# Kernel optimization log

Hardware: AMD Instinct MI355X
Metric: run time of the kernel (lower is better)

The kernel has to match this reference:

```python
import jax, jax.numpy as jnp
import numpy as np
import math

EPS_LN = 1e-5
TARGET_ACTIVITY = 0.1
THETA = 2.0 ** 16

B, NH, T, D, N = 2, 12, 2048, 768, 256


def layernorm(x):
    m = jnp.mean(x, axis=-1, keepdims=True)
    v = jnp.mean((x - m) ** 2, axis=-1, keepdims=True)
    return (x - m) / jnp.sqrt(v + EPS_LN)


def get_freqs(n):
    q = jnp.floor(jnp.arange(n, dtype=jnp.float32) / 2.0) * 2.0  # quantize by 2
    return 1.0 / (THETA ** (q / n)) / (2.0 * math.pi)


def rope(phases, v):
    ph = (phases % 1.0) * (2.0 * math.pi)
    c, s = jnp.cos(ph), jnp.sin(ph)
    even = v[..., 0::2]
    odd = v[..., 1::2]
    v_rot = jnp.stack((-odd, even), axis=-1).reshape(v.shape)  # interleaved rotate
    return v * c + v_rot * s


def setup_inputs() -> dict:
    key = jax.random.key(0)
    ks = jax.random.split(key, 5)
    std = 0.02
    return {
        "x": jax.random.normal(ks[0], (B, 1, T, D), dtype=jnp.float32),
        "encoder": jax.random.normal(ks[1], (NH, D, N), dtype=jnp.float32) * std,
        "encoder_v": jax.random.normal(ks[2], (NH, D, N), dtype=jnp.float32) * std,
        "decoder": jax.random.normal(ks[3], (NH * N, D), dtype=jnp.float32) * std,
        "scale": jnp.ones((D,), dtype=jnp.float32),
        "running_activity": jnp.ones((D,), dtype=jnp.float32) * TARGET_ACTIVITY,
    }


def reference(x, encoder, encoder_v, decoder, scale, running_activity):
    Bv, _, Tv, Dv = x.shape
    nh, _, Nv = encoder.shape

    # encode + ReLU sparsify: [B,1,T,D] @ [nh,D,N] -> [B,nh,T,N]
    x_latent = jnp.einsum('bztd,hdn->bhtn', x, encoder)
    x_sparse = jax.nn.relu(x_latent)

    # RoPE on Q=K=x_sparse
    freqs = get_freqs(Nv)  # [N]
    r_phases = jnp.arange(Tv, dtype=jnp.float32)[:, None] * freqs[None, :]  # [T,N]
    QR = rope(r_phases, x_sparse)
    KR = rope(r_phases, x_sparse)

    # non-softmax causal attention, strictly lower-triangular (diag=-1)
    scores = jnp.einsum('bhtn,bhsn->bhts', QR, KR)
    mask = jnp.tril(jnp.ones((Tv, Tv), dtype=scores.dtype), k=-1)
    scores = scores * mask
    yKV = jnp.einsum('bhts,bsd->bhtd', scores, x[:, 0])  # V = x

    yKV = layernorm(yKV)
    y_sparse = jax.nn.relu(jnp.einsum('bhtd,hdn->bhtn', yKV, encoder_v))
    xy_sparse = x_sparse * y_sparse  # [B,nh,T,N]; dropout=0 (eval)

    # [B,nh,T,N] -> [B,1,T,nh*N] @ [nh*N,D]
    flat = jnp.transpose(xy_sparse, (0, 2, 1, 3)).reshape(Bv, 1, Tv, nh * Nv)
    yMLP = flat @ decoder

    y = layernorm(yMLP)
    regulation = TARGET_ACTIVITY / (running_activity + 1e-6)
    y = y * jnp.sqrt(regulation) * scale

    return layernorm(x + y), xy_sparse
```

## Files before the change

kernel.cpp:

```cpp
#include <hip/hip_runtime.h>
#include <math.h>

#define TT 2048
#define DD 768
#define NN 256
#define NHH 12
#define BB 2
#define CH 512

typedef unsigned short u16;
typedef __attribute__((ext_vector_type(8))) short bf16x8;
typedef __attribute__((ext_vector_type(8))) unsigned short u16x8;
typedef __attribute__((ext_vector_type(4))) float f32x4;

static inline int imin(int a, int b) { return a < b ? a : b; }

__device__ __forceinline__ u16 f2b(float f) {
  union { float f; unsigned u; } a; a.f = f;
  unsigned r = a.u + 0x7FFF + ((a.u >> 16) & 1);
  return (u16)(r >> 16);
}
__device__ __forceinline__ float b2f(u16 h) {
  union { unsigned u; float f; } a; a.u = ((unsigned)h) << 16;
  return a.f;
}

__device__ __forceinline__ void async16(const void* g, void* l) {
  __builtin_amdgcn_global_load_lds(
      (const __attribute__((address_space(1))) unsigned*)g,
      (__attribute__((address_space(3))) unsigned*)l, 16, 0, 0);
}

__device__ __forceinline__ void stage128x32(
    const u16* __restrict__ gbase, size_t ld, u16* lds, int tid) {
  const int w = tid >> 6, l = tid & 63;
  const int r = l >> 2, kc = (l & 3) << 3;
#pragma unroll
  for (int q = 0; q < 2; ++q) {
    const int row0 = w * 32 + q * 16;
    async16(gbase + (size_t)(row0 + r) * ld + kc, lds + row0 * 32);
  }
}

__device__ __forceinline__ void stage64x32(
    const u16* __restrict__ gbase, size_t ld, u16* lds, int tid) {
  const int w = tid >> 6, l = tid & 63;
  const int r = w * 16 + (l >> 2), kc = (l & 3) << 3;
  async16(gbase + (size_t)r * ld + kc, lds + w * 512);
}

__device__ __forceinline__ void mfma_step(
    const u16* As, const u16* Bs, int wr, int wc, int lane, f32x4 acc[4][4]) {
  const int m16 = lane & 15, quad = lane >> 4;
  bf16x8 a[4], b[4];
#pragma unroll
  for (int i = 0; i < 4; ++i)
    a[i] = *(const bf16x8*)&As[(wr * 64 + i * 16 + m16) * 32 + quad * 8];
#pragma unroll
  for (int j = 0; j < 4; ++j)
    b[j] = *(const bf16x8*)&Bs[(wc * 64 + j * 16 + m16) * 32 + quad * 8];
#pragma unroll
  for (int i = 0; i < 4; ++i)
#pragma unroll
    for (int j = 0; j < 4; ++j)
      acc[i][j] = __builtin_amdgcn_mfma_f32_16x16x32_bf16(a[i], b[j], acc[i][j], 0, 0, 0);
}

__device__ __forceinline__ void copy_out64(
    const u16* buf, u16* g, size_t ld, int tid) {
#pragma unroll
  for (int s = 0; s < 4; ++s) {
    const int off = (s * 256 + tid) * 8;
    const int row = off >> 7, col = off & 127;
    *(u16x8*)&g[(size_t)row * ld + col] = *(const u16x8*)&buf[off];
  }
}

#define GEMM_PROLOGUE()                                            \
  __shared__ __attribute__((aligned(16))) u16 smem[16384];         \
  const int tid = threadIdx.x;                                     \
  const int w = tid >> 6, lane = tid & 63;                         \
  const int wr = w >> 1, wc = w & 1;                               \
  const int col16 = lane & 15, quad = lane >> 4;                   \
  f32x4 acc[4][4];                                                 \
  _Pragma("unroll") for (int i = 0; i < 4; ++i)                    \
  _Pragma("unroll") for (int j = 0; j < 4; ++j)                    \
      acc[i][j] = (f32x4){0.f, 0.f, 0.f, 0.f};

#define PIPELINED_K_LOOP(ABASE, ALD, BBASE, BLD, KTOT)                      \
  {                                                                         \
    u16* bA_ = smem; u16* bB_ = smem + 8192;                                \
    stage128x32((ABASE), (ALD), bA_, tid);                                  \
    stage128x32((BBASE), (BLD), bA_ + 4096, tid);                           \
    const int nk_ = (KTOT) / 32;                                            \
    for (int kp_ = 0; kp_ < nk_; ++kp_) {                                   \
      u16* cb_ = (kp_ & 1) ? bB_ : bA_;                                     \
      u16* nb_ = (kp_ & 1) ? bA_ : bB_;                                     \
      if (kp_ + 1 < nk_) {                                                  \
        const int kn_ = (kp_ + 1) * 32;                                     \
        stage128x32((ABASE) + kn_, (ALD), nb_, tid);                        \
        stage128x32((BBASE) + kn_, (BLD), nb_ + 4096, tid);                 \
        asm volatile("s_waitcnt vmcnt(4)" ::: "memory");                    \
      } else {                                                              \
        asm volatile("s_waitcnt vmcnt(0)" ::: "memory");                    \
      }                                                                     \
      __builtin_amdgcn_s_barrier();                                         \
      __builtin_amdgcn_sched_barrier(0);                                    \
      mfma_step(cb_, cb_ + 4096, wr, wc, lane, acc);                        \
      __builtin_amdgcn_sched_barrier(0);                                    \
      __builtin_amdgcn_s_barrier();                                         \
    }                                                                       \
  }

__global__ __launch_bounds__(256) void cvt_bf16(
    const float* __restrict__ in, u16* __restrict__ out, size_t n4) {
  size_t i = ((size_t)blockIdx.x * 256 + threadIdx.x) * 4;
  if (i >= n4 * 4) return;
  float4 v = *(const float4*)&in[i];
  u16 o[4] = {f2b(v.x), f2b(v.y), f2b(v.z), f2b(v.w)};
  *(ushort4*)&out[i] = *(ushort4*)o;
}

__global__ __launch_bounds__(256) void tcvt_bf16(
    const float* __restrict__ in, u16* __restrict__ out, int R, int C,
    size_t inStride, size_t outStride) {
  __shared__ float tile[32][33];
  const float* ip = in + (size_t)blockIdx.z * inStride;
  u16* op = out + (size_t)blockIdx.z * outStride;
  const int c0 = blockIdx.x * 32, r0 = blockIdx.y * 32;
  const int tx = threadIdx.x & 31, ty = threadIdx.x >> 5;
#pragma unroll
  for (int p = 0; p < 4; ++p)
    tile[ty + p * 8][tx] = ip[(size_t)(r0 + ty + p * 8) * C + c0 + tx];
  __syncthreads();
#pragma unroll
  for (int p = 0; p < 4; ++p)
    op[(size_t)(c0 + ty + p * 8) * R + r0 + tx] = f2b(tile[tx][ty + p * 8]);
}

__global__ __launch_bounds__(256) void k_colsum(
    const u16* __restrict__ encvt, float* __restrict__ colsum) {
  const int row = blockIdx.x * 4 + (threadIdx.x >> 6);
  const int lane = threadIdx.x & 63;
  const u16* pr = encvt + (size_t)row * DD;
  float s = 0.f;
#pragma unroll
  for (int i = 0; i < 3; ++i) {
    ushort4 v = *(const ushort4*)&pr[(lane << 2) + i * 256];
    s += b2f(v.x) + b2f(v.y) + b2f(v.z) + b2f(v.w);
  }
#pragma unroll
  for (int off = 32; off; off >>= 1) s += __shfl_xor(s, off);
  if (lane == 0) colsum[row] = s;
}

__global__ __launch_bounds__(256) void k1_encode(
    const u16* __restrict__ x16, const u16* __restrict__ enct,
    u16* __restrict__ qr16, u16* __restrict__ qrt16) {
  const int h = blockIdx.z;
  const int m0 = blockIdx.x * 128, n0 = blockIdx.y * 128;
  GEMM_PROLOGUE();
  PIPELINED_K_LOOP(x16 + (size_t)m0 * DD, DD,
                   enct + ((size_t)h * NN + n0) * DD, DD, DD);
#pragma unroll
  for (int p = 0; p < 2; ++p) {
    __syncthreads();
    if (wr == p) {
#pragma unroll
      for (int i = 0; i < 4; ++i)
#pragma unroll
        for (int j = 0; j < 4; ++j) {
          const int n = n0 + wc * 64 + j * 16 + col16;
          const int q = n & ~1;
          const float freq = exp2f((float)q * -0.0625f) * 0.15915494309189535f;
          float rv[4], pv[4];
#pragma unroll
          for (int r = 0; r < 4; ++r) rv[r] = fmaxf(acc[i][j][r], 0.f);
#pragma unroll
          for (int r = 0; r < 4; ++r) pv[r] = __shfl_xor(rv[r], 1);
#pragma unroll
          for (int r = 0; r < 4; ++r) {
            const int lr = i * 16 + quad * 4 + r;
            const int t = (m0 + p * 64 + lr) & (TT - 1);
            float phase = (float)t * freq;
            float ph = (phase - floorf(phase)) * 6.283185307179586f;
            float s = __sinf(ph), c = __cosf(ph);
            float o = (n & 1) ? (rv[r] * c + pv[r] * s) : (rv[r] * c - pv[r] * s);
            smem[lr * 128 + wc * 64 + j * 16 + col16] = f2b(o);
          }
        }
    }
    __syncthreads();
    const int m = m0 + p * 64;
    const int b = m >> 11, tb = m & (TT - 1);
    const size_t sl = (size_t)(b * NHH + h);
    copy_out64(smem, qr16 + (sl * TT + tb) * NN + n0, NN, tid);
#pragma unroll
    for (int s = 0; s < 4; ++s) {
      const int off = (s * 256 + tid) * 8;
      const int nr = off >> 6, tc = off & 63;
      u16 vals[8];
#pragma unroll
      for (int k = 0; k < 8; ++k) vals[k] = smem[(tc + k) * 128 + nr];
      *(u16x8*)&qrt16[(sl * NN + n0 + nr) * TT + tb + tc] = *(u16x8*)vals;
    }
  }
}

__global__ __launch_bounds__(256) void kS_band(
    const u16* __restrict__ qr16, u16* __restrict__ sb, int bh0) {
  const int z = blockIdx.y;
  const int bh = bh0 + z;
  const int cc = blockIdx.x / 10, rr = blockIdx.x % 10;
  int i = (int)((sqrtf(8.f * rr + 1.f) - 1.f) * 0.5f);
  while ((i + 1) * (i + 2) / 2 <= rr) ++i;
  while (i * (i + 1) / 2 > rr) --i;
  const int j = rr - i * (i + 1) / 2;
  const int t0 = (cc * 4 + i) * 128;
  const int s0 = cc * CH + j * 128;
  const u16* q = qr16 + (size_t)bh * TT * NN;
  GEMM_PROLOGUE();
  PIPELINED_K_LOOP(q + (size_t)t0 * NN, NN, q + (size_t)s0 * NN, NN, NN);
  const bool diag = (i == j);
#pragma unroll
  for (int p = 0; p < 2; ++p) {
    __syncthreads();
    if (wr == p) {
#pragma unroll
      for (int ii = 0; ii < 4; ++ii)
#pragma unroll
        for (int jj = 0; jj < 4; ++jj) {
          const int s = s0 + wc * 64 + jj * 16 + col16;
#pragma unroll
          for (int r = 0; r < 4; ++r) {
            const int lr = ii * 16 + quad * 4 + r;
            const int t = t0 + p * 64 + lr;
            float v = acc[ii][jj][r];
            if (diag && s >= t) v = 0.f;
            smem[lr * 128 + wc * 64 + jj * 16 + col16] = f2b(v);
          }
        }
    }
    __syncthreads();
    copy_out64(smem, sb + ((size_t)z * TT + t0 + p * 64) * CH + j * 128, CH, tid);
  }
}

__global__ __launch_bounds__(256) void kB_all(
    const u16* __restrict__ xt16, const u16* __restrict__ qrt16,
    u16* __restrict__ h16, int bh0) {
  __shared__ __attribute__((aligned(16))) u16 sm[20480];
  u16* buf0 = sm;
  u16* buf1 = sm + 6144;
  u16* snap = sm + 12288;
  const int tid = threadIdx.x;
  const int w = tid >> 6, lane = tid & 63;
  const int m16 = lane & 15, quad = lane >> 4;
  const int z = blockIdx.z;
  const int bh = bh0 + z, b = bh / NHH;
  const int d0 = blockIdx.x * 64, n0 = blockIdx.y * 128;
  f32x4 acc[4][2];
#pragma unroll
  for (int i = 0; i < 4; ++i)
#pragma unroll
    for (int j = 0; j < 2; ++j) acc[i][j] = (f32x4){0.f, 0.f, 0.f, 0.f};
  const u16* Ab = xt16 + ((size_t)b * DD + d0) * TT;
  const u16* Bb = qrt16 + ((size_t)bh * NN + n0) * TT;
  for (int c = 0; c < 3; ++c) {
    const int kbase = c * CH;
    stage64x32(Ab + kbase, TT, buf0, tid);
    stage128x32(Bb + kbase, TT, buf0 + 2048, tid);
    for (int s = 0; s < CH / 32; ++s) {
      u16* cb = (s & 1) ? buf1 : buf0;
      u16* nb = (s & 1) ? buf0 : buf1;
      if (s + 1 < CH / 32) {
        const int kn = kbase + (s + 1) * 32;
        stage64x32(Ab + kn, TT, nb, tid);
        stage128x32(Bb + kn, TT, nb + 2048, tid);
        asm volatile("s_waitcnt vmcnt(3)" ::: "memory");
      } else {
        asm volatile("s_waitcnt vmcnt(0)" ::: "memory");
      }
      __builtin_amdgcn_s_barrier();
      __builtin_amdgcn_sched_barrier(0);
      bf16x8 a[4], bb[2];
#pragma unroll
      for (int i = 0; i < 4; ++i)
        a[i] = *(const bf16x8*)&cb[(i * 16 + m16) * 32 + quad * 8];
#pragma unroll
      for (int j = 0; j < 2; ++j)
        bb[j] = *(const bf16x8*)&cb[2048 + (w * 32 + j * 16 + m16) * 32 + quad * 8];
#pragma unroll
      for (int i = 0; i < 4; ++i)
#pragma unroll
        for (int j = 0; j < 2; ++j)
          acc[i][j] = __builtin_amdgcn_mfma_f32_16x16x32_bf16(a[i], bb[j], acc[i][j], 0, 0, 0);
      __builtin_amdgcn_sched_barrier(0);
      __builtin_amdgcn_s_barrier();
    }
#pragma unroll
    for (int i = 0; i < 4; ++i)
#pragma unroll
      for (int j = 0; j < 2; ++j)
#pragma unroll
        for (int r = 0; r < 4; ++r)
          snap[(i * 16 + quad * 4 + r) * 128 + w * 32 + j * 16 + m16] =
              f2b(acc[i][j][r]);
    __syncthreads();
    u16* hd = h16 + (size_t)(z * 3 + c) * DD * NN;
#pragma unroll
    for (int s4 = 0; s4 < 4; ++s4) {
      const int off = (s4 * 256 + tid) * 8;
      const int row = off >> 7, col = off & 127;
      *(u16x8*)&hd[(size_t)(d0 + row) * NN + n0 + col] = *(const u16x8*)&snap[off];
    }
    __syncthreads();
  }
}

__device__ static const int TTORD[16] = {15, 11, 7, 14, 10, 6, 13, 9,
                                         5, 3, 12, 8, 4, 2, 1, 0};

__global__ __launch_bounds__(256) void kA_attn(
    const u16* __restrict__ qr16, const u16* __restrict__ h16,
    const u16* __restrict__ sb, const u16* __restrict__ xt16,
    u16* __restrict__ ykv16, int bh0) {
  __shared__ __attribute__((aligned(16))) u16 smem[32768];
  const int tid = threadIdx.x;
  const int w = tid >> 6, lane = tid & 63;
  const int wr = w >> 1, wc = w & 1;
  const int col16 = lane & 15, quad = lane >> 4;
  const int nwg = gridDim.x;
  const int bid = blockIdx.x;
  const int qq = nwg >> 3, r8 = nwg & 7;
  const int xcd = bid & 7, pos = bid >> 3;
  const int wg = (xcd < r8 ? xcd * (qq + 1) : r8 * (qq + 1) + (xcd - r8) * qq) + pos;
  const int z = wg / 96;
  const int tt = TTORD[(wg / 6) & 15];
  const int d0 = (wg % 6) * 128;
  const int bh = bh0 + z, b = bh / NHH;
  const int c = tt >> 2, it = tt & 3;
  const int t0 = tt * 128;
  f32x4 acc[4][4];
#pragma unroll
  for (int i = 0; i < 4; ++i)
#pragma unroll
    for (int j = 0; j < 4; ++j) acc[i][j] = (f32x4){0.f, 0.f, 0.f, 0.f};

  const int c4 = (c > 0) ? 4 : 0;
  const int nP = c4 + (it + 1) * 2;
  const u16* hs = h16 + ((size_t)(z * 3 + (c > 0 ? c - 1 : 0)) * DD + d0) * NN;
  const u16* qb = qr16 + ((size_t)bh * TT + t0) * NN;
  const u16* sbb = sb + ((size_t)z * TT + t0) * CH;
  const u16* xb = xt16 + ((size_t)b * DD + d0) * TT + c * CH;

#define KA_STAGE(buf, p)                                                  \
  {                                                                       \
    const u16 *pa_, *pb_; size_t la_, lb_;                                \
    if ((p) < c4) {                                                       \
      pa_ = qb + (p) * 64; la_ = NN;                                      \
      pb_ = hs + (p) * 64; lb_ = NN;                                      \
    } else {                                                              \
      const int q_ = (p) - c4;                                            \
      const int j_ = q_ >> 1, kk_ = (q_ & 1) << 6;                        \
      pa_ = sbb + j_ * 128 + kk_; la_ = CH;                               \
      pb_ = xb + j_ * 128 + kk_; lb_ = TT;                                \
    }                                                                     \
    stage128x32(pa_, la_, (buf), tid);                                    \
    stage128x32(pa_ + 32, la_, (buf) + 4096, tid);                        \
    stage128x32(pb_, lb_, (buf) + 8192, tid);                             \
    stage128x32(pb_ + 32, lb_, (buf) + 12288, tid);                       \
  }

  u16* bufA = smem;
  u16* bufB = smem + 16384;
  KA_STAGE(bufA, 0);
  for (int p = 0; p < nP; ++p) {
    u16* cb = (p & 1) ? bufB : bufA;
    u16* nb = (p & 1) ? bufA : bufB;
    if (p + 1 < nP) {
      KA_STAGE(nb, p + 1);
      asm volatile("s_waitcnt vmcnt(8)" ::: "memory");
    } else {
      asm volatile("s_waitcnt vmcnt(0)" ::: "memory");
    }
    __builtin_amdgcn_s_barrier();
    __builtin_amdgcn_sched_barrier(0);
    mfma_step(cb, cb + 8192, wr, wc, lane, acc);
    mfma_step(cb + 4096, cb + 12288, wr, wc, lane, acc);
    __builtin_amdgcn_sched_barrier(0);
    __builtin_amdgcn_s_barrier();
  }
#undef KA_STAGE

#pragma unroll
  for (int p = 0; p < 2; ++p) {
    __syncthreads();
    if (wr == p) {
#pragma unroll
      for (int i = 0; i < 4; ++i)
#pragma unroll
        for (int j = 0; j < 4; ++j)
#pragma unroll
          for (int r = 0; r < 4; ++r) {
            const int lr = i * 16 + quad * 4 + r;
            smem[lr * 128 + wc * 64 + j * 16 + col16] = f2b(acc[i][j][r]);
          }
    }
    __syncthreads();
    copy_out64(smem, ykv16 + ((size_t)z * TT + t0 + p * 64) * DD + d0, DD, tid);
  }
}

__global__ __launch_bounds__(256) void k3_stats(
    const u16* __restrict__ ykv16, float* __restrict__ mu, float* __restrict__ rs) {
  const int row = blockIdx.x * 4 + (threadIdx.x >> 6);
  const int lane = threadIdx.x & 63;
  const u16* p = ykv16 + (size_t)row * DD;
  float sum = 0.f, sq = 0.f;
#pragma unroll
  for (int i = 0; i < 3; ++i) {
    ushort4 v = *(const ushort4*)&p[(lane << 2) + i * 256];
    float f0 = b2f(v.x), f1 = b2f(v.y), f2 = b2f(v.z), f3 = b2f(v.w);
    sum += f0 + f1 + f2 + f3;
    sq += f0 * f0 + f1 * f1 + f2 * f2 + f3 * f3;
  }
#pragma unroll
  for (int off = 32; off; off >>= 1) {
    sum += __shfl_xor(sum, off);
    sq += __shfl_xor(sq, off);
  }
  if (lane == 0) {
    float m = sum * (1.f / 768.f);
    float v = sq * (1.f / 768.f) - m * m;
    mu[row] = m;
    rs[row] = rsqrtf(v + 1e-5f);
  }
}

__global__ __launch_bounds__(256) void k4_xy(
    const u16* __restrict__ ykv16, const u16* __restrict__ encvt,
    u16* __restrict__ qrxy, const float* __restrict__ mu,
    const float* __restrict__ rs, const float* __restrict__ colsum,
    float* __restrict__ out2, int bh0) {
  const int z = blockIdx.z;
  const int bh = bh0 + z, h = bh % NHH;
  const int t0 = blockIdx.x * 128, n0 = blockIdx.y * 128;
  GEMM_PROLOGUE();
  PIPELINED_K_LOOP(ykv16 + ((size_t)z * TT + t0) * DD, DD,
                   encvt + ((size_t)h * NN + n0) * DD, DD, DD);
#pragma unroll
  for (int p = 0; p < 2; ++p) {
    __syncthreads();
    if (wr == p) {
#pragma unroll
      for (int i = 0; i < 4; ++i)
#pragma unroll
        for (int j = 0; j < 4; ++j) {
          const int n = n0 + wc * 64 + j * 16 + col16;
          const int qn = n & ~1;
          const float freq = exp2f((float)qn * -0.0625f) * 0.15915494309189535f;
          const float cs = colsum[h * NN + n];
#pragma unroll
          for (int r = 0; r < 4; ++r) {
            const int lr = i * 16 + quad * 4 + r;
            const int t = t0 + p * 64 + lr;
            const int lrow = z * TT + t;
            const float muv = mu[lrow], rsv = rs[lrow];
            float ys = fmaxf(rsv * acc[i][j][r] - rsv * muv * cs, 0.f);
            const size_t gi = ((size_t)bh * TT + t) * NN + n;
            float qs = b2f(qrxy[gi]);
            float qp = b2f(qrxy[gi ^ 1]);
            float phase = (float)t * freq;
            float ph = (phase - floorf(phase)) * 6.283185307179586f;
            float s = __sinf(ph), c2 = __cosf(ph);
            float xs = (n & 1) ? (qs * c2 - qp * s) : (qs * c2 + qp * s);
            float val = ys * xs;
            out2[gi] = val;
            smem[lr * 128 + wc * 64 + j * 16 + col16] = f2b(val);
          }
        }
    }
    __syncthreads();
    copy_out64(smem, qrxy + ((size_t)bh * TT + t0 + p * 64) * NN + n0, NN, tid);
  }
}

__global__ __launch_bounds__(256) void k5_mlp(
    const u16* __restrict__ xyq, const u16* __restrict__ dect,
    float* __restrict__ ymlp) {
  __shared__ __attribute__((aligned(16))) u16 sm[8192];
  u16* buf0 = sm;
  u16* buf1 = sm + 4096;
  const int tid = threadIdx.x;
  const int w = tid >> 6, lane = tid & 63;
  const int wr = w >> 1, wc = w & 1;
  const int m16 = lane & 15, quad = lane >> 4;
  const int m0 = blockIdx.x * 64, d0 = blockIdx.y * 64;
  f32x4 acc[2][2];
#pragma unroll
  for (int i = 0; i < 2; ++i)
#pragma unroll
    for (int j = 0; j < 2; ++j) acc[i][j] = (f32x4){0.f, 0.f, 0.f, 0.f};
  const int ar = w * 16 + (lane >> 2);
  const int m = m0 + ar;
  const int b = m >> 11, t = m & (TT - 1);
  const int kc = (lane & 3) << 3;
  const int NK = NHH * NN / 32;
  async16(xyq + ((size_t)(b * NHH) * TT + t) * NN + kc, buf0 + w * 512);
  stage64x32(dect + (size_t)d0 * (NHH * NN), NHH * NN, buf0 + 2048, tid);
  for (int s = 0; s < NK; ++s) {
    u16* cb = (s & 1) ? buf1 : buf0;
    u16* nb = (s & 1) ? buf0 : buf1;
    if (s + 1 < NK) {
      const int k0 = (s + 1) * 32;
      const int hh = k0 >> 8;
      const int kk = (k0 & 255) + kc;
      async16(xyq + ((size_t)(b * NHH + hh) * TT + t) * NN + kk, nb + w * 512);
      stage64x32(dect + (size_t)d0 * (NHH * NN) + k0, NHH * NN, nb + 2048, tid);
      asm volatile("s_waitcnt vmcnt(2)" ::: "memory");
    } else {
      asm volatile("s_waitcnt vmcnt(0)" ::: "memory");
    }
    __builtin_amdgcn_s_barrier();
    __builtin_amdgcn_sched_barrier(0);
    bf16x8 a[2], bb[2];
#pragma unroll
    for (int i = 0; i < 2; ++i)
      a[i] = *(const bf16x8*)&cb[(wr * 32 + i * 16 + m16) * 32 + quad * 8];
#pragma unroll
    for (int j = 0; j < 2; ++j)
      bb[j] = *(const bf16x8*)&cb[2048 + (wc * 32 + j * 16 + m16) * 32 + quad * 8];
#pragma unroll
    for (int i = 0; i < 2; ++i)
#pragma unroll
      for (int j = 0; j < 2; ++j)
        acc[i][j] = __builtin_amdgcn_mfma_f32_16x16x32_bf16(a[i], bb[j], acc[i][j], 0, 0, 0);
    __builtin_amdgcn_sched_barrier(0);
    __builtin_amdgcn_s_barrier();
  }
#pragma unroll
  for (int i = 0; i < 2; ++i)
#pragma unroll
    for (int j = 0; j < 2; ++j) {
      const int d = d0 + wc * 32 + j * 16 + m16;
#pragma unroll
      for (int r = 0; r < 4; ++r) {
        const int mm = m0 + wr * 32 + i * 16 + quad * 4 + r;
        ymlp[(size_t)mm * DD + d] = acc[i][j][r];
      }
    }
}

__global__ __launch_bounds__(256) void k6_final(
    const float* __restrict__ ymlp, const float* __restrict__ x,
    const float* __restrict__ scale, const float* __restrict__ ra,
    float* __restrict__ out1) {
  const int row = blockIdx.x;
  const int tid = threadIdx.x;
  const int wid = tid >> 6, lane = tid & 63;
  __shared__ float red[8];
  float v[3];
  float sum = 0.f, sq = 0.f;
#pragma unroll
  for (int j = 0; j < 3; ++j) {
    v[j] = ymlp[(size_t)row * DD + tid + j * 256];
    sum += v[j]; sq += v[j] * v[j];
  }
#pragma unroll
  for (int off = 32; off; off >>= 1) { sum += __shfl_xor(sum, off); sq += __shfl_xor(sq, off); }
  if (lane == 0) { red[wid] = sum; red[4 + wid] = sq; }
  __syncthreads();
  sum = red[0] + red[1] + red[2] + red[3];
  sq = red[4] + red[5] + red[6] + red[7];
  const float m1 = sum * (1.f / 768.f);
  const float r1 = rsqrtf(sq * (1.f / 768.f) - m1 * m1 + 1e-5f);
  float z[3];
  float sum2 = 0.f, sq2 = 0.f;
#pragma unroll
  for (int j = 0; j < 3; ++j) {
    const int d = tid + j * 256;
    float y = (v[j] - m1) * r1 * sqrtf(0.1f / (ra[d] + 1e-6f)) * scale[d];
    z[j] = x[(size_t)row * DD + d] + y;
    sum2 += z[j]; sq2 += z[j] * z[j];
  }
  __syncthreads();
#pragma unroll
  for (int off = 32; off; off >>= 1) { sum2 += __shfl_xor(sum2, off); sq2 += __shfl_xor(sq2, off); }
  if (lane == 0) { red[wid] = sum2; red[4 + wid] = sq2; }
  __syncthreads();
  sum2 = red[0] + red[1] + red[2] + red[3];
  sq2 = red[4] + red[5] + red[6] + red[7];
  const float m2 = sum2 * (1.f / 768.f);
  const float r2 = rsqrtf(sq2 * (1.f / 768.f) - m2 * m2 + 1e-5f);
#pragma unroll
  for (int j = 0; j < 3; ++j)
    out1[(size_t)row * DD + tid + j * 256] = (z[j] - m2) * r2;
}

extern "C" void kernel_launch(void* const* d_in, const int* in_sizes, int n_in,
                              void* d_out, int out_size, void* d_ws, size_t ws_size,
                              hipStream_t stream) {
  const float* x = (const float*)d_in[0];
  const float* enc = (const float*)d_in[1];
  const float* encv = (const float*)d_in[2];
  const float* dec = (const float*)d_in[3];
  const float* scale = (const float*)d_in[4];
  const float* ra = (const float*)d_in[5];
  float* out1 = (float*)d_out;
  float* out2 = out1 + (size_t)BB * TT * DD;
  float* ymlp = out1;

  const int NS = BB * NHH;
  unsigned char* p = (unsigned char*)d_ws;
  u16* X16 = (u16*)p;    p += (size_t)BB * TT * DD * 2;
  u16* XT16 = (u16*)p;   p += (size_t)BB * DD * TT * 2;
  u16* ENCT = (u16*)p;   p += (size_t)NHH * NN * DD * 2;
  u16* ENCVT = (u16*)p;  p += (size_t)NHH * NN * DD * 2;
  u16* DECT = (u16*)p;   p += (size_t)DD * NHH * NN * 2;
  u16* QR16 = (u16*)p;   p += (size_t)NS * TT * NN * 2;
  u16* QRT16 = (u16*)p;  p += (size_t)NS * NN * TT * 2;
  float* COLSUM = (float*)p; p += (size_t)NHH * NN * 4;
  const size_t SLICE_B = (size_t)TT * CH * 2 + 3 * (size_t)DD * NN * 2 +
                         (size_t)TT * DD * 2 + (size_t)TT * 8;
  size_t fixed = (size_t)(p - (unsigned char*)d_ws);
  size_t rem = (ws_size > fixed) ? ws_size - fixed : 0;
  int GSmax = (int)(rem / SLICE_B);
  if (GSmax < 1) GSmax = 1;
  if (GSmax > NS) GSmax = NS;
  const int ngrp = (NS + GSmax - 1) / GSmax;
  const int GS = (NS + ngrp - 1) / ngrp;
  u16* SB = (u16*)p;     p += (size_t)GS * TT * CH * 2;
  u16* H16 = (u16*)p;    p += (size_t)GS * 3 * DD * NN * 2;
  u16* YKV16 = (u16*)p;  p += (size_t)GS * TT * DD * 2;
  float* MU = (float*)p; p += (size_t)GS * TT * 4;
  float* RS = (float*)p; p += (size_t)GS * TT * 4;

  cvt_bf16<<<dim3((BB * TT * DD) / 1024), 256, 0, stream>>>(x, X16, (size_t)BB * TT * DD / 4);
  tcvt_bf16<<<dim3(DD / 32, TT / 32, BB), 256, 0, stream>>>(
      x, XT16, TT, DD, (size_t)TT * DD, (size_t)DD * TT);
  tcvt_bf16<<<dim3(NN / 32, DD / 32, NHH), 256, 0, stream>>>(
      enc, ENCT, DD, NN, (size_t)DD * NN, (size_t)NN * DD);
  tcvt_bf16<<<dim3(NN / 32, DD / 32, NHH), 256, 0, stream>>>(
      encv, ENCVT, DD, NN, (size_t)DD * NN, (size_t)NN * DD);
  tcvt_bf16<<<dim3(DD / 32, (NHH * NN) / 32, 1), 256, 0, stream>>>(
      dec, DECT, NHH * NN, DD, 0, 0);
  k_colsum<<<dim3(NHH * NN / 4), 256, 0, stream>>>(ENCVT, COLSUM);

  k1_encode<<<dim3(BB * TT / 128, NN / 128, NHH), 256, 0, stream>>>(
      X16, ENCT, QR16, QRT16);

  for (int bh0 = 0; bh0 < NS; bh0 += GS) {
    const int gs = imin(GS, NS - bh0);
    kS_band<<<dim3(40, gs), 256, 0, stream>>>(QR16, SB, bh0);
    kB_all<<<dim3(DD / 64, NN / 128, gs), 256, 0, stream>>>(
        XT16, QRT16, H16, bh0);
    kA_attn<<<dim3(96 * gs), 256, 0, stream>>>(
        QR16, H16, SB, XT16, YKV16, bh0);
    k3_stats<<<dim3(gs * TT / 4), 256, 0, stream>>>(YKV16, MU, RS);
    k4_xy<<<dim3(TT / 128, NN / 128, gs), 256, 0, stream>>>(
        YKV16, ENCVT, QR16, MU, RS, COLSUM, out2, bh0);
  }

  k5_mlp<<<dim3(BB * TT / 64, DD / 64), 256, 0, stream>>>(QR16, DECT, ymlp);
  k6_final<<<dim3(BB * TT), 256, 0, stream>>>(ymlp, x, scale, ra, out1);
}
```

Before: 409.7 us.

## Precompute RoPE cos/sin table, single-pass epilogues, and K=64 staging in MLP GEMM

Adds a kernel that precomputes a cos/sin table per (t, pair). The encode and xy kernels now read this table instead of evaluating exp2/sin/cos per element. The two-pass half-tile epilogues in several GEMM kernels become one full 128-row smem pass with a single copy-out, which removes extra barriers. The MLP GEMM now stages 64-wide K chunks per iteration to halve the number of loop iterations and barriers. Other changes: packed pair loads of QR in k4 and hoisted mu/rs loads. The costs are one extra small kernel and a larger LDS footprint in k5.

```diff
diff --git a/kernel.cpp b/kernel.cpp
--- a/kernel.cpp
+++ b/kernel.cpp
@@ -66,10 +66,10 @@
       acc[i][j] = __builtin_amdgcn_mfma_f32_16x16x32_bf16(a[i], b[j], acc[i][j], 0, 0, 0);
 }
 
-__device__ __forceinline__ void copy_out64(
+__device__ __forceinline__ void copy_out128(
     const u16* buf, u16* g, size_t ld, int tid) {
 #pragma unroll
-  for (int s = 0; s < 4; ++s) {
+  for (int s = 0; s < 8; ++s) {
     const int off = (s * 256 + tid) * 8;
     const int row = off >> 7, col = off & 127;
     *(u16x8*)&g[(size_t)row * ld + col] = *(const u16x8*)&buf[off];
@@ -154,56 +154,57 @@
   if (lane == 0) colsum[row] = s;
 }
 
+__global__ __launch_bounds__(256) void k_cstab(float2* __restrict__ cs) {
+  const int idx = blockIdx.x * 256 + threadIdx.x;
+  const int t = idx >> 7, n2 = idx & 127;
+  const float freq = exp2f((float)(2 * n2) * -0.0625f) * 0.15915494309189535f;
+  const float phase = (float)t * freq;
+  const float ph = (phase - floorf(phase)) * 6.283185307179586f;
+  cs[idx] = make_float2(__cosf(ph), __sinf(ph));
+}
+
 __global__ __launch_bounds__(256) void k1_encode(
     const u16* __restrict__ x16, const u16* __restrict__ enct,
+    const float2* __restrict__ CS,
     u16* __restrict__ qr16, u16* __restrict__ qrt16) {
   const int h = blockIdx.z;
   const int m0 = blockIdx.x * 128, n0 = blockIdx.y * 128;
   GEMM_PROLOGUE();
   PIPELINED_K_LOOP(x16 + (size_t)m0 * DD, DD,
                    enct + ((size_t)h * NN + n0) * DD, DD, DD);
-#pragma unroll
-  for (int p = 0; p < 2; ++p) {
-    __syncthreads();
-    if (wr == p) {
-#pragma unroll
-      for (int i = 0; i < 4; ++i)
-#pragma unroll
-        for (int j = 0; j < 4; ++j) {
-          const int n = n0 + wc * 64 + j * 16 + col16;
-          const int q = n & ~1;
-          const float freq = exp2f((float)q * -0.0625f) * 0.15915494309189535f;
-          float rv[4], pv[4];
-#pragma unroll
-          for (int r = 0; r < 4; ++r) rv[r] = fmaxf(acc[i][j][r], 0.f);
-#pragma unroll
-          for (int r = 0; r < 4; ++r) pv[r] = __shfl_xor(rv[r], 1);
-#pragma unroll
-          for (int r = 0; r < 4; ++r) {
-            const int lr = i * 16 + quad * 4 + r;
-            const int t = (m0 + p * 64 + lr) & (TT - 1);
-            float phase = (float)t * freq;
-            float ph = (phase - floorf(phase)) * 6.283185307179586f;
-            float s = __sinf(ph), c = __cosf(ph);
-            float o = (n & 1) ? (rv[r] * c + pv[r] * s) : (rv[r] * c - pv[r] * s);
-            smem[lr * 128 + wc * 64 + j * 16 + col16] = f2b(o);
-          }
-        }
-    }
-    __syncthreads();
-    const int m = m0 + p * 64;
-    const int b = m >> 11, tb = m & (TT - 1);
-    const size_t sl = (size_t)(b * NHH + h);
-    copy_out64(smem, qr16 + (sl * TT + tb) * NN + n0, NN, tid);
-#pragma unroll
-    for (int s = 0; s < 4; ++s) {
-      const int off = (s * 256 + tid) * 8;
-      const int nr = off >> 6, tc = off & 63;
-      u16 vals[8];
-#pragma unroll
-      for (int k = 0; k < 8; ++k) vals[k] = smem[(tc + k) * 128 + nr];
-      *(u16x8*)&qrt16[(sl * NN + n0 + nr) * TT + tb + tc] = *(u16x8*)vals;
-    }
+  __syncthreads();
+#pragma unroll
+  for (int i = 0; i < 4; ++i)
+#pragma unroll
+    for (int j = 0; j < 4; ++j) {
+      const int n = n0 + wc * 64 + j * 16 + col16;
+      float rv[4], pv[4];
+#pragma unroll
+      for (int r = 0; r < 4; ++r) rv[r] = fmaxf(acc[i][j][r], 0.f);
+#pragma unroll
+      for (int r = 0; r < 4; ++r) pv[r] = __shfl_xor(rv[r], 1);
+#pragma unroll
+      for (int r = 0; r < 4; ++r) {
+        const int lrow = wr * 64 + i * 16 + quad * 4 + r;
+        const int t = (m0 + lrow) & (TT - 1);
+        const float2 cs = CS[t * 128 + (n >> 1)];
+        const float o = (n & 1) ? (rv[r] * cs.x + pv[r] * cs.y)
+                                : (rv[r] * cs.x - pv[r] * cs.y);
+        smem[lrow * 128 + wc * 64 + j * 16 + col16] = f2b(o);
+      }
+    }
+  __syncthreads();
+  const int bq = m0 >> 11, tb = m0 & (TT - 1);
+  const size_t sl = (size_t)(bq * NHH + h);
+  copy_out128(smem, qr16 + (sl * TT + tb) * NN + n0, NN, tid);
+#pragma unroll
+  for (int s = 0; s < 8; ++s) {
+    const int off = (s * 256 + tid) * 8;
+    const int nr = off >> 7, tc = off & 127;
+    u16 vals[8];
+#pragma unroll
+    for (int k = 0; k < 8; ++k) vals[k] = smem[(tc + k) * 128 + nr];
+    *(u16x8*)&qrt16[(sl * NN + n0 + nr) * TT + tb + tc] = *(u16x8*)vals;
   }
 }
 
@@ -222,28 +223,23 @@
   GEMM_PROLOGUE();
   PIPELINED_K_LOOP(q + (size_t)t0 * NN, NN, q + (size_t)s0 * NN, NN, NN);
   const bool diag = (i == j);
-#pragma unroll
-  for (int p = 0; p < 2; ++p) {
-    __syncthreads();
-    if (wr == p) {
-#pragma unroll
-      for (int ii = 0; ii < 4; ++ii)
-#pragma unroll
-        for (int jj = 0; jj < 4; ++jj) {
-          const int s = s0 + wc * 64 + jj * 16 + col16;
-#pragma unroll
-          for (int r = 0; r < 4; ++r) {
-            const int lr = ii * 16 + quad * 4 + r;
-            const int t = t0 + p * 64 + lr;
-            float v = acc[ii][jj][r];
-            if (diag && s >= t) v = 0.f;
-            smem[lr * 128 + wc * 64 + jj * 16 + col16] = f2b(v);
-          }
-        }
-    }
-    __syncthreads();
-    copy_out64(smem, sb + ((size_t)z * TT + t0 + p * 64) * CH + j * 128, CH, tid);
-  }
+  __syncthreads();
+#pragma unroll
+  for (int ii = 0; ii < 4; ++ii)
+#pragma unroll
+    for (int jj = 0; jj < 4; ++jj) {
+      const int s = s0 + wc * 64 + jj * 16 + col16;
+#pragma unroll
+      for (int r = 0; r < 4; ++r) {
+        const int lrow = wr * 64 + ii * 16 + quad * 4 + r;
+        const int t = t0 + lrow;
+        float v = acc[ii][jj][r];
+        if (diag && s >= t) v = 0.f;
+        smem[lrow * 128 + wc * 64 + jj * 16 + col16] = f2b(v);
+      }
+    }
+  __syncthreads();
+  copy_out128(smem, sb + ((size_t)z * TT + t0) * CH + j * 128, CH, tid);
 }
 
 __global__ __launch_bounds__(256) void kB_all(
@@ -393,23 +389,18 @@
   }
 #undef KA_STAGE
 
-#pragma unroll
-  for (int p = 0; p < 2; ++p) {
-    __syncthreads();
-    if (wr == p) {
-#pragma unroll
-      for (int i = 0; i < 4; ++i)
-#pragma unroll
-        for (int j = 0; j < 4; ++j)
-#pragma unroll
-          for (int r = 0; r < 4; ++r) {
-            const int lr = i * 16 + quad * 4 + r;
-            smem[lr * 128 + wc * 64 + j * 16 + col16] = f2b(acc[i][j][r]);
-          }
-    }
-    __syncthreads();
-    copy_out64(smem, ykv16 + ((size_t)z * TT + t0 + p * 64) * DD + d0, DD, tid);
-  }
+  __syncthreads();
+#pragma unroll
+  for (int i = 0; i < 4; ++i)
+#pragma unroll
+    for (int j = 0; j < 4; ++j)
+#pragma unroll
+      for (int r = 0; r < 4; ++r) {
+        const int lrow = wr * 64 + i * 16 + quad * 4 + r;
+        smem[lrow * 128 + wc * 64 + j * 16 + col16] = f2b(acc[i][j][r]);
+      }
+  __syncthreads();
+  copy_out128(smem, ykv16 + ((size_t)z * TT + t0) * DD + d0, DD, tid);
 }
 
 __global__ __launch_bounds__(256) void k3_stats(
@@ -440,6 +431,7 @@
 
 __global__ __launch_bounds__(256) void k4_xy(
     const u16* __restrict__ ykv16, const u16* __restrict__ encvt,
+    const float2* __restrict__ CS,
     u16* __restrict__ qrxy, const float* __restrict__ mu,
     const float* __restrict__ rs, const float* __restrict__ colsum,
     float* __restrict__ out2, int bh0) {
@@ -449,49 +441,47 @@
   GEMM_PROLOGUE();
   PIPELINED_K_LOOP(ykv16 + ((size_t)z * TT + t0) * DD, DD,
                    encvt + ((size_t)h * NN + n0) * DD, DD, DD);
-#pragma unroll
-  for (int p = 0; p < 2; ++p) {
-    __syncthreads();
-    if (wr == p) {
-#pragma unroll
-      for (int i = 0; i < 4; ++i)
-#pragma unroll
-        for (int j = 0; j < 4; ++j) {
-          const int n = n0 + wc * 64 + j * 16 + col16;
-          const int qn = n & ~1;
-          const float freq = exp2f((float)qn * -0.0625f) * 0.15915494309189535f;
-          const float cs = colsum[h * NN + n];
-#pragma unroll
-          for (int r = 0; r < 4; ++r) {
-            const int lr = i * 16 + quad * 4 + r;
-            const int t = t0 + p * 64 + lr;
-            const int lrow = z * TT + t;
-            const float muv = mu[lrow], rsv = rs[lrow];
-            float ys = fmaxf(rsv * acc[i][j][r] - rsv * muv * cs, 0.f);
-            const size_t gi = ((size_t)bh * TT + t) * NN + n;
-            float qs = b2f(qrxy[gi]);
-            float qp = b2f(qrxy[gi ^ 1]);
-            float phase = (float)t * freq;
-            float ph = (phase - floorf(phase)) * 6.283185307179586f;
-            float s = __sinf(ph), c2 = __cosf(ph);
-            float xs = (n & 1) ? (qs * c2 - qp * s) : (qs * c2 + qp * s);
-            float val = ys * xs;
-            out2[gi] = val;
-            smem[lr * 128 + wc * 64 + j * 16 + col16] = f2b(val);
-          }
-        }
-    }
-    __syncthreads();
-    copy_out64(smem, qrxy + ((size_t)bh * TT + t0 + p * 64) * NN + n0, NN, tid);
-  }
+  __syncthreads();
+#pragma unroll
+  for (int i = 0; i < 4; ++i) {
+    float muv[4], rsv[4];
+#pragma unroll
+    for (int r = 0; r < 4; ++r) {
+      const int lrow = z * TT + t0 + wr * 64 + i * 16 + quad * 4 + r;
+      muv[r] = mu[lrow];
+      rsv[r] = rs[lrow];
+    }
+#pragma unroll
+    for (int j = 0; j < 4; ++j) {
+      const int n = n0 + wc * 64 + j * 16 + col16;
+      const float csum = colsum[h * NN + n];
+#pragma unroll
+      for (int r = 0; r < 4; ++r) {
+        const int lrow = wr * 64 + i * 16 + quad * 4 + r;
+        const int t = t0 + lrow;
+        const float ys = fmaxf(rsv[r] * acc[i][j][r] - rsv[r] * muv[r] * csum, 0.f);
+        const size_t gi = ((size_t)bh * TT + t) * NN + n;
+        const unsigned pq = *(const unsigned*)&qrxy[gi & ~(size_t)1];
+        const float lo = b2f((u16)pq), hi = b2f((u16)(pq >> 16));
+        const float2 cs = CS[t * 128 + (n >> 1)];
+        const float xs = (n & 1) ? (hi * cs.x - lo * cs.y)
+                                 : (lo * cs.x + hi * cs.y);
+        const float val = ys * xs;
+        out2[gi] = val;
+        smem[lrow * 128 + wc * 64 + j * 16 + col16] = f2b(val);
+      }
+    }
+  }
+  __syncthreads();
+  copy_out128(smem, qrxy + ((size_t)bh * TT + t0) * NN + n0, NN, tid);
 }
 
 __global__ __launch_bounds__(256) void k5_mlp(
     const u16* __restrict__ xyq, const u16* __restrict__ dect,
     float* __restrict__ ymlp) {
-  __shared__ __attribute__((aligned(16))) u16 sm[8192];
+  __shared__ __attribute__((aligned(16))) u16 sm[16384];
   u16* buf0 = sm;
-  u16* buf1 = sm + 4096;
+  u16* buf1 = sm + 8192;
   const int tid = threadIdx.x;
   const int w = tid >> 6, lane = tid & 63;
   const int wr = w >> 1, wc = w & 1;
@@ -506,39 +496,50 @@
   const int m = m0 + ar;
   const int b = m >> 11, t = m & (TT - 1);
   const int kc = (lane & 3) << 3;
-  const int NK = NHH * NN / 32;
-  async16(xyq + ((size_t)(b * NHH) * TT + t) * NN + kc, buf0 + w * 512);
-  stage64x32(dect + (size_t)d0 * (NHH * NN), NHH * NN, buf0 + 2048, tid);
+#define K5_STAGE(buf, k0)                                                   \
+  {                                                                         \
+    const int hh_ = (k0) >> 8;                                              \
+    const int kk_ = ((k0) & 255) + kc;                                      \
+    const u16* ap_ = xyq + ((size_t)(b * NHH + hh_) * TT + t) * NN;         \
+    async16(ap_ + kk_, (buf) + w * 512);                                    \
+    async16(ap_ + kk_ + 32, (buf) + 2048 + w * 512);                        \
+    stage64x32(dect + (size_t)d0 * (NHH * NN) + (k0), NHH * NN,             \
+               (buf) + 4096, tid);                                          \
+    stage64x32(dect + (size_t)d0 * (NHH * NN) + (k0) + 32, NHH * NN,        \
+               (buf) + 6144, tid);                                          \
+  }
+  const int NK = (NHH * NN) / 64;
+  K5_STAGE(buf0, 0);
   for (int s = 0; s < NK; ++s) {
     u16* cb = (s & 1) ? buf1 : buf0;
     u16* nb = (s & 1) ? buf0 : buf1;
     if (s + 1 < NK) {
-      const int k0 = (s + 1) * 32;
-      const int hh = k0 >> 8;
-      const int kk = (k0 & 255) + kc;
-      async16(xyq + ((size_t)(b * NHH + hh) * TT + t) * NN + kk, nb + w * 512);
-      stage64x32(dect + (size_t)d0 * (NHH * NN) + k0, NHH * NN, nb + 2048, tid);
-      asm volatile("s_waitcnt vmcnt(2)" ::: "memory");
+      K5_STAGE(nb, (s + 1) * 64);
+      asm volatile("s_waitcnt vmcnt(4)" ::: "memory");
     } else {
       asm volatile("s_waitcnt vmcnt(0)" ::: "memory");
     }
     __builtin_amdgcn_s_barrier();
     __builtin_amdgcn_sched_barrier(0);
-    bf16x8 a[2], bb[2];
-#pragma unroll
-    for (int i = 0; i < 2; ++i)
-      a[i] = *(const bf16x8*)&cb[(wr * 32 + i * 16 + m16) * 32 + quad * 8];
-#pragma unroll
-    for (int j = 0; j < 2; ++j)
-      bb[j] = *(const bf16x8*)&cb[2048 + (wc * 32 + j * 16 + m16) * 32 + quad * 8];
-#pragma unroll
-    for (int i = 0; i < 2; ++i)
+#pragma unroll
+    for (int half = 0; half < 2; ++half) {
+      bf16x8 a[2], bb[2];
+#pragma unroll
+      for (int i = 0; i < 2; ++i)
+        a[i] = *(const bf16x8*)&cb[half * 2048 + (wr * 32 + i * 16 + m16) * 32 + quad * 8];
 #pragma unroll
       for (int j = 0; j < 2; ++j)
-        acc[i][j] = __builtin_amdgcn_mfma_f32_16x16x32_bf16(a[i], bb[j], acc[i][j], 0, 0, 0);
+        bb[j] = *(const bf16x8*)&cb[4096 + half * 2048 + (wc * 32 + j * 16 + m16) * 32 + quad * 8];
+#pragma unroll
+      for (int i = 0; i < 2; ++i)
+#pragma unroll
+        for (int j = 0; j < 2; ++j)
+          acc[i][j] = __builtin_amdgcn_mfma_f32_16x16x32_bf16(a[i], bb[j], acc[i][j], 0, 0, 0);
+    }
     __builtin_amdgcn_sched_barrier(0);
     __builtin_amdgcn_s_barrier();
   }
+#undef K5_STAGE
 #pragma unroll
   for (int i = 0; i < 2; ++i)
 #pragma unroll
@@ -621,6 +622,7 @@
   u16* QR16 = (u16*)p;   p += (size_t)NS * TT * NN * 2;
   u16* QRT16 = (u16*)p;  p += (size_t)NS * NN * TT * 2;
   float* COLSUM = (float*)p; p += (size_t)NHH * NN * 4;
+  float2* CS = (float2*)p;   p += (size_t)TT * (NN / 2) * sizeof(float2);
   const size_t SLICE_B = (size_t)TT * CH * 2 + 3 * (size_t)DD * NN * 2 +
                          (size_t)TT * DD * 2 + (size_t)TT * 8;
   size_t fixed = (size_t)(p - (unsigned char*)d_ws);
@@ -646,9 +648,10 @@
   tcvt_bf16<<<dim3(DD / 32, (NHH * NN) / 32, 1), 256, 0, stream>>>(
       dec, DECT, NHH * NN, DD, 0, 0);
   k_colsum<<<dim3(NHH * NN / 4), 256, 0, stream>>>(ENCVT, COLSUM);
+  k_cstab<<<dim3(TT * (NN / 2) / 256), 256, 0, stream>>>(CS);
 
   k1_encode<<<dim3(BB * TT / 128, NN / 128, NHH), 256, 0, stream>>>(
-      X16, ENCT, QR16, QRT16);
+      X16, ENCT, CS, QR16, QRT16);
 
   for (int bh0 = 0; bh0 < NS; bh0 += GS) {
     const int gs = imin(GS, NS - bh0);
@@ -659,7 +662,7 @@
         QR16, H16, SB, XT16, YKV16, bh0);
     k3_stats<<<dim3(gs * TT / 4), 256, 0, stream>>>(YKV16, MU, RS);
     k4_xy<<<dim3(TT / 128, NN / 128, gs), 256, 0, stream>>>(
-        YKV16, ENCVT, QR16, MU, RS, COLSUM, out2, bh0);
+        YKV16, ENCVT, CS, QR16, MU, RS, COLSUM, out2, bh0);
   }
 
   k5_mlp<<<dim3(BB * TT / 64, DD / 64), 256, 0, stream>>>(QR16, DECT, ymlp);
```

Result: no change. 402.3 us (-1.8%).
